# Performance work log

Measured on AMD Instinct MI355X. Metric: run time of the kernel, lower is better.

The kernel has to match this reference:

```python
import jax, jax.numpy as jnp
import numpy as np

DK = 128  # key/query head dim (also value dim)

def setup_inputs() -> dict:
    key = jax.random.key(0)
    k1, k2, k3, k4 = jax.random.split(key, 4)
    query = jax.random.normal(k1, (8, 512, 28, 28), dtype=jnp.float32)
    support = jax.random.normal(k2, (16, 512, 28, 28), dtype=jnp.float32)
    Wk = jax.random.normal(k3, (128, 512), dtype=jnp.float32) * (1.0 / np.sqrt(512.0))
    Wv = jax.random.normal(k4, (128, 512), dtype=jnp.float32) * (1.0 / np.sqrt(512.0))
    return {"query": query, "support": support, "Wk": Wk, "Wv": Wv}

def reference(query, support, Wk, Wv):
    B, D, H, W = query.shape
    N, Ds, Hs, Ws = support.shape
    q_flat = query.reshape(B, D, H * W)        # b d u
    s_flat = support.reshape(N, Ds, Hs * Ws)   # n d v
    # 1x1 convs == channel projections (query_head is aliased to key_head)
    q = jnp.einsum('kd,bdu->bku', Wk, q_flat)            # B dk u
    query_value = jnp.einsum('kd,bdu->bku', Wv, q_flat)  # B dv u
    support_key = jnp.einsum('kd,ndv->nkv', Wk, s_flat)  # N dk v
    support_value = jnp.einsum('kd,ndv->nkv', Wv, s_flat)  # N dv v
    scores = jnp.einsum('bku,nkv->bnuv', q, support_key) / jnp.sqrt(jnp.float32(DK))
    # first softmax over dim=3 in the source is dead code (overwritten); effective
    # attention is softmax over the support-class axis n (dim=1)
    attn = jax.nn.softmax(scores, axis=1)  # B N u v
    # note: u is summed out here, exactly as in the source einsum
    query_aligned = jnp.einsum('bnuv,nkv->bkv', attn, support_value)  # B dv v
    a = query_aligned.transpose(0, 2, 1)   # B v dv
    b = query_value.transpose(0, 2, 1)     # B u dv
    # cdist(p=2)**2 == squared euclidean distances; compute without forming diffs
    a2 = jnp.sum(a * a, axis=-1)  # B v
    b2 = jnp.sum(b * b, axis=-1)  # B u
    ab = jnp.einsum('bpd,brd->bpr', a, b)  # B v u
    d2 = jnp.maximum(a2[:, :, None] + b2[:, None, :] - 2.0 * ab, 0.0)
    P, R = d2.shape[1], d2.shape[2]
    return jnp.sum(d2, axis=(1, 2)) / (P * R)  # (B,)
```

## Files before the change

kernel.cpp:

```cpp
#include <hip/hip_runtime.h>

#define U_CNT 784
#define DKH   128
#define DD    512
#define NS    16

typedef short bf16x8 __attribute__((ext_vector_type(8)));
typedef float f32x4  __attribute__((ext_vector_type(4)));

__device__ __forceinline__ unsigned short f2bf(float f) {
  unsigned u = __builtin_bit_cast(unsigned, f);
  u += 0x7fffu + ((u >> 16) & 1u);
  return (unsigned short)(u >> 16);
}

__device__ __forceinline__ float rowg_sum(float x) {
  float a, b;
  asm("v_mov_b32 %0, %2\n\t"
      "v_mov_b32 %1, %2\n\t"
      "v_permlane16_swap_b32 %0, %1"
      : "=&v"(a), "=&v"(b) : "v"(x));
  float s = a + b;
  float c, d;
  asm("v_mov_b32 %0, %2\n\t"
      "v_mov_b32 %1, %2\n\t"
      "v_permlane32_swap_b32 %0, %1"
      : "=&v"(c), "=&v"(d) : "v"(s));
  return c + d;
}


__global__ __launch_bounds__(256)
void cast_w(const float* __restrict__ Wk, const float* __restrict__ Wv,
            unsigned short* __restrict__ Wkv_f) {
  int g = blockIdx.x * 256 + threadIdx.x;
  int fidx = g >> 6, l = g & 63;
  int f = fidx >> 4, rd = (fidx >> 2) & 3, ds = fidx & 3;
  int row = f * 16 + (l & 15);
  int dbase = rd * 128 + ds * 32 + (l >> 4) * 8;
  const float* src = (row < 128) ? (Wk + row * DD + dbase) : (Wv + (row - 128) * DD + dbase);
  unsigned short* dst = Wkv_f + (size_t)fidx * 512 + l * 8;
#pragma unroll
  for (int j = 0; j < 8; ++j) dst[j] = f2bf(src[j]);
}

__global__ __launch_bounds__(256, 1)
void proj_kernel(const float* __restrict__ query, const float* __restrict__ support,
                 const unsigned short* __restrict__ Wkv_f,
                 unsigned short* __restrict__ q_f, unsigned short* __restrict__ sk_f,
                 float* __restrict__ sv_t, float* __restrict__ S1p, float* __restrict__ S2p) {
  constexpr int PB = 112;
  constexpr int DR = 128;
  constexpr int RW = DR + 8;
  __shared__ __align__(16) unsigned short xs[2][PB * RW];
  int pc = blockIdx.x;
  int m  = blockIdx.y;
  int tid = threadIdx.x;
  int p0 = pc * PB;
  const float* X = (m < 8) ? (query + (size_t)m * DD * U_CNT)
                           : (support + (size_t)(m - 8) * DD * U_CNT);
  int drow = tid >> 1, pg = tid & 1;
  const float* xrow = X + p0 + pg * 4;

  float4 vbuf[14];
  auto loadR = [&](int rd) {
    const float* s = xrow + (size_t)(rd * DR + drow) * U_CNT;
#pragma unroll
    for (int i = 0; i < 14; ++i) vbuf[i] = *(const float4*)(s + i * 8);
  };
  auto storeR = [&](int bb) {
    unsigned short* d0 = &xs[bb][(pg * 4) * RW + drow];
#pragma unroll
    for (int i = 0; i < 14; ++i) {
      unsigned short* dp = d0 + (i * 8) * RW;
      dp[0]      = f2bf(vbuf[i].x); dp[RW]     = f2bf(vbuf[i].y);
      dp[2 * RW] = f2bf(vbuf[i].z); dp[3 * RW] = f2bf(vbuf[i].w);
    }
  };

  int wave = tid >> 6, l = tid & 63;
  int col = l & 15, rowg = l >> 4;

  f32x4 acc[7][4];
  f32x4 zero = {0.f, 0.f, 0.f, 0.f};
#pragma unroll
  for (int v7 = 0; v7 < 7; ++v7)
#pragma unroll
    for (int rr = 0; rr < 4; ++rr) acc[v7][rr] = zero;

  loadR(0); storeR(0);
  __syncthreads();
  for (int rd = 0; rd < 4; ++rd) {
    if (rd < 3) loadR(rd + 1);
    int bb = rd & 1;
#pragma unroll
    for (int ds = 0; ds < 4; ++ds) {
      int dl = ds * 32 + rowg * 8;
      bf16x8 Af[4];
#pragma unroll
      for (int rr = 0; rr < 4; ++rr)
        Af[rr] = *(const bf16x8*)(Wkv_f +
                 (size_t)((((wave * 4 + rr) * 4 + rd) * 4 + ds) * 512) + l * 8);
#pragma unroll
      for (int v7 = 0; v7 < 7; ++v7) {
        bf16x8 bf = *(const bf16x8*)(&xs[bb][(v7 * 16 + col) * RW + dl]);
#pragma unroll
        for (int rr = 0; rr < 4; ++rr)
          acc[v7][rr] = __builtin_amdgcn_mfma_f32_16x16x32_bf16(Af[rr], bf, acc[v7][rr], 0, 0, 0);
      }
    }
    if (rd < 3) {
      __syncthreads();
      storeR((rd + 1) & 1);
      __syncthreads();
    }
  }

  if (m < 8) {
    if (wave < 2) {
#pragma unroll
      for (int rr = 0; rr < 4; ++rr) {
        int r = wave * 4 + rr;
        const float sc = 0.08838834764831845f * 1.4426950408889634f;
#pragma unroll
        for (int v7 = 0; v7 < 7; ++v7) {
          ushort4 o;
          o.x = f2bf(acc[v7][rr][0] * sc); o.y = f2bf(acc[v7][rr][1] * sc);
          o.z = f2bf(acc[v7][rr][2] * sc); o.w = f2bf(acc[v7][rr][3] * sc);
          size_t off = (size_t)m * 100352 + (size_t)(pc * 7 + v7) * 2048 +
                       (size_t)(2 * r + (rowg >> 1)) * 128 + col * 8 + (rowg & 1) * 4;
          *(ushort4*)(q_f + off) = o;
        }
      }
    } else {
      float s1 = 0.f;
#pragma unroll
      for (int rr = 0; rr < 4; ++rr) {
        int r = wave * 4 + rr;
#pragma unroll
        for (int j = 0; j < 4; ++j) {
          float xsum = 0.f;
#pragma unroll
          for (int v7 = 0; v7 < 7; ++v7) {
            float x = acc[v7][rr][j];
            s1 += x * x; xsum += x;
          }
          xsum += __shfl_xor(xsum, 1, 64); xsum += __shfl_xor(xsum, 2, 64);
          xsum += __shfl_xor(xsum, 4, 64); xsum += __shfl_xor(xsum, 8, 64);
          if (col == 0)
            S2p[((size_t)pc * 8 + m) * DKH + (r - 8) * 16 + rowg * 4 + j] = xsum;
        }
      }
#pragma unroll
      for (int o = 32; o >= 1; o >>= 1) s1 += __shfl_xor(s1, o, 64);
      if (l == 0) S1p[((wave - 2) * 7 + pc) * 8 + m] = s1;
    }
  } else {
    int img = m - 8;
    if (wave < 2) {
#pragma unroll
      for (int rr = 0; rr < 4; ++rr) {
        int r = wave * 4 + rr;
#pragma unroll
        for (int v7 = 0; v7 < 7; ++v7) {
          ushort4 o;
          o.x = f2bf(acc[v7][rr][0]); o.y = f2bf(acc[v7][rr][1]);
          o.z = f2bf(acc[v7][rr][2]); o.w = f2bf(acc[v7][rr][3]);
          size_t off = (size_t)(p0 + v7 * 16 + col) * 2048 +
                       (size_t)(2 * r + (rowg >> 1)) * 128 + img * 8 + (rowg & 1) * 4;
          *(ushort4*)(sk_f + off) = o;
        }
      }
    } else {
#pragma unroll
      for (int rr = 0; rr < 4; ++rr) {
        int r = wave * 4 + rr;
        int kb = (r - 8) * 16 + rowg * 4;
#pragma unroll
        for (int v7 = 0; v7 < 7; ++v7) {
          int p = p0 + v7 * 16 + col;
          float4 o = make_float4(acc[v7][rr][0], acc[v7][rr][1], acc[v7][rr][2], acc[v7][rr][3]);
          *(float4*)(sv_t + (size_t)(img * U_CNT + p) * DKH + kb) = o;
        }
      }
    }
  }
}

__global__ __launch_bounds__(256, 3)
void score_kernel(const unsigned short* __restrict__ q_f,
                  const unsigned short* __restrict__ sk_f,
                  float* __restrict__ w_part) {
  int bx = blockIdx.x;
  int b  = bx & 7;
  int inner = bx >> 3;
  int uc = inner / 49;
  int vb = inner - uc * 49;
  int wv = threadIdx.x >> 6;
  int l  = threadIdx.x & 63;
  int col = l & 15, rowg = l >> 4;
  int vbase = vb * 16 + wv * 4;

  bf16x8 A[4][4];
#pragma unroll
  for (int v = 0; v < 4; ++v) {
    const unsigned short* ap = sk_f + (size_t)(vbase + v) * 2048 + rowg * 128 + col * 8;
#pragma unroll
    for (int s = 0; s < 4; ++s) A[v][s] = *(const bf16x8*)(ap + s * 512);
  }

  float wl[4][4];
#pragma unroll
  for (int v = 0; v < 4; ++v)
#pragma unroll
    for (int j = 0; j < 4; ++j) wl[v][j] = 0.f;

  int ut0 = (uc == 0) ? 0 : uc * 12 + 1;
  int cnt = (uc == 0) ? 13 : 12;
  const unsigned short* qb = q_f + (size_t)b * 100352 + rowg * 128 + col * 8;
  f32x4 zero = {0.f, 0.f, 0.f, 0.f};

  const unsigned short* qp0 = qb + (size_t)ut0 * 2048;
  bf16x8 B0 = *(const bf16x8*)(qp0);
  bf16x8 B1 = *(const bf16x8*)(qp0 + 512);
  bf16x8 B2 = *(const bf16x8*)(qp0 + 1024);
  bf16x8 B3 = *(const bf16x8*)(qp0 + 1536);

  for (int it = 0; it < cnt; ++it) {
    int nit = (it + 1 < cnt) ? it + 1 : it;
    const unsigned short* qp = qb + (size_t)(ut0 + nit) * 2048;
    bf16x8 N0 = *(const bf16x8*)(qp);
    bf16x8 N1 = *(const bf16x8*)(qp + 512);
    bf16x8 N2 = *(const bf16x8*)(qp + 1024);
    bf16x8 N3 = *(const bf16x8*)(qp + 1536);

    f32x4 acc[4];
#pragma unroll
    for (int v = 0; v < 4; ++v)
      acc[v] = __builtin_amdgcn_mfma_f32_16x16x32_bf16(A[v][0], B0, zero, 0, 0, 0);
#pragma unroll
    for (int v = 0; v < 4; ++v)
      acc[v] = __builtin_amdgcn_mfma_f32_16x16x32_bf16(A[v][1], B1, acc[v], 0, 0, 0);
#pragma unroll
    for (int v = 0; v < 4; ++v)
      acc[v] = __builtin_amdgcn_mfma_f32_16x16x32_bf16(A[v][2], B2, acc[v], 0, 0, 0);
#pragma unroll
    for (int v = 0; v < 4; ++v)
      acc[v] = __builtin_amdgcn_mfma_f32_16x16x32_bf16(A[v][3], B3, acc[v], 0, 0, 0);

    float e[4][4], ps[4];
#pragma unroll
    for (int v = 0; v < 4; ++v) {
      e[v][0] = __builtin_amdgcn_exp2f(acc[v][0]);
      e[v][1] = __builtin_amdgcn_exp2f(acc[v][1]);
      e[v][2] = __builtin_amdgcn_exp2f(acc[v][2]);
      e[v][3] = __builtin_amdgcn_exp2f(acc[v][3]);
      ps[v] = (e[v][0] + e[v][1]) + (e[v][2] + e[v][3]);
    }
#pragma unroll
    for (int v = 0; v < 4; ++v) ps[v] = rowg_sum(ps[v]);
#pragma unroll
    for (int v = 0; v < 4; ++v) {
      float r = __builtin_amdgcn_rcpf(ps[v]);
      wl[v][0] += e[v][0] * r; wl[v][1] += e[v][1] * r;
      wl[v][2] += e[v][2] * r; wl[v][3] += e[v][3] * r;
    }
    B0 = N0; B1 = N1; B2 = N2; B3 = N3;
  }
#pragma unroll
  for (int v = 0; v < 4; ++v)
#pragma unroll
    for (int j = 0; j < 4; ++j) {
      float x = wl[v][j];
      x += __shfl_xor(x, 1, 64); x += __shfl_xor(x, 2, 64);
      x += __shfl_xor(x, 4, 64); x += __shfl_xor(x, 8, 64);
      wl[v][j] = x;
    }
  __shared__ float wst[4][4][16];
#pragma unroll
  for (int v = 0; v < 4; ++v)
    if (col == v) {
#pragma unroll
      for (int j = 0; j < 4; ++j) wst[wv][v][rowg * 4 + j] = wl[v][j];
    }
  __syncthreads();
  int t = threadIdx.x;
  int vl = t >> 4, c = t & 15;
  w_part[(((size_t)uc * 8 + b) * U_CNT + vb * 16 + vl) * NS + c] =
      wst[vl >> 2][vl & 3][c];
}

__global__ __launch_bounds__(256)
void align_kernel(const float* __restrict__ w_part, const float* __restrict__ sv_t,
                  float* __restrict__ T1p, float* __restrict__ T2p) {
  int vt2 = blockIdx.x;
  int t = threadIdx.x;
  __shared__ float w_sh[2][8][16];
  {
    int vl = t >> 7, b = (t >> 4) & 7, n = t & 15;
    float s = 0.f;
#pragma unroll
    for (int uc = 0; uc < 4; ++uc)
      s += w_part[(((size_t)uc * 8 + b) * U_CNT + vt2 * 2 + vl) * NS + n];
    w_sh[vl][b][n] = s;
  }
  __syncthreads();
  int k = t & 127, vl = t >> 7;
  int v = vt2 * 2 + vl;
  float a[8];
#pragma unroll
  for (int b = 0; b < 8; ++b) a[b] = 0.f;
#pragma unroll
  for (int n = 0; n < NS; ++n) {
    float s = sv_t[((size_t)n * U_CNT + v) * DKH + k];
#pragma unroll
    for (int b = 0; b < 8; ++b) a[b] += w_sh[vl][b][n] * s;
  }
  __shared__ float red[8][128];
  if (vl == 1) {
#pragma unroll
    for (int b = 0; b < 8; ++b) red[b][k] = a[b];
  }
  __syncthreads();
  if (vl == 0) {
#pragma unroll
    for (int b = 0; b < 8; ++b)
      T2p[((size_t)vt2 * 8 + b) * DKH + k] = a[b] + red[b][k];
  }
  __shared__ float sw1[4][8];
#pragma unroll
  for (int b = 0; b < 8; ++b) {
    float x = a[b] * a[b];
#pragma unroll
    for (int o = 32; o >= 1; o >>= 1) x += __shfl_xor(x, o, 64);
    if ((t & 63) == 0) sw1[t >> 6][b] = x;
  }
  __syncthreads();
  if (t < 8) T1p[vt2 * 8 + t] = sw1[0][t] + sw1[1][t] + sw1[2][t] + sw1[3][t];
}

__global__ __launch_bounds__(256)
void reduce_partials(const float* __restrict__ S1p, const float* __restrict__ T1p,
                     const float* __restrict__ S2p, const float* __restrict__ T2p,
                     float* __restrict__ S2, float* __restrict__ T2,
                     float* __restrict__ ST1) {
  __shared__ float smem[264];
  int bx = blockIdx.x, t = threadIdx.x;
  if (bx < 32) {
    int b = bx >> 2, kq = bx & 3;
    int kl = t & 31, g = t >> 5;
    int k = kq * 32 + kl;
    float s = 0.f;
    for (int w = g; w < 392; w += 8)
      s += T2p[((size_t)w * 8 + b) * DKH + k];
    smem[g * 32 + kl] = s;
    __syncthreads();
    if (t < 32) {
      float v = 0.f;
#pragma unroll
      for (int g2 = 0; g2 < 8; ++g2) v += smem[g2 * 32 + t];
      T2[b * DKH + kq * 32 + t] = v;
    }
  } else {
    int b = bx - 32;
    int k = t & 127, h = t >> 7;
    float s = 0.f;
    for (int w = h; w < 7; w += 2)
      s += S2p[((size_t)w * 8 + b) * DKH + k];
    if (h == 1) smem[k] = s;
    __syncthreads();
    if (h == 0) S2[b * DKH + k] = s + smem[k];
    float c = 0.f;
    for (int i = t; i < 14; i += 256)  c += S1p[i * 8 + b];
    for (int i = t; i < 392; i += 256) c += T1p[i * 8 + b];
#pragma unroll
    for (int o = 32; o >= 1; o >>= 1) c += __shfl_xor(c, o, 64);
    if ((t & 63) == 0) smem[256 + (t >> 6)] = c;
    __syncthreads();
    if (t == 0) ST1[b] = smem[256] + smem[257] + smem[258] + smem[259];
  }
}

__global__ void final_kernel(const float* __restrict__ S2, const float* __restrict__ T2,
                             const float* __restrict__ ST1, float* __restrict__ out) {
  int b = blockIdx.x, t = threadIdx.x;
  float p = S2[b * DKH + t] * T2[b * DKH + t];
#pragma unroll
  for (int o = 32; o >= 1; o >>= 1) p += __shfl_xor(p, o, 64);
  __shared__ float s2[2];
  if ((t & 63) == 0) s2[t >> 6] = p;
  __syncthreads();
  if (t == 0)
    out[b] = (784.0f * ST1[b] - 2.0f * (s2[0] + s2[1])) * (1.0f / (784.0f * 784.0f));
}

extern "C" void kernel_launch(void* const* d_in, const int* in_sizes, int n_in,
                              void* d_out, int out_size, void* d_ws, size_t ws_size,
                              hipStream_t stream) {
  const float* query   = (const float*)d_in[0];
  const float* support = (const float*)d_in[1];
  const float* Wk      = (const float*)d_in[2];
  const float* Wv      = (const float*)d_in[3];
  float* out = (float*)d_out;
  char* ws = (char*)d_ws;

  unsigned short* Wkv  = (unsigned short*)(ws + 0);
  unsigned short* q_f  = (unsigned short*)(ws + 262144);
  unsigned short* sk_f = (unsigned short*)(ws + 1867776);
  float*          sv_t = (float*)(ws + 5079040);
  float*          w_part = (float*)(ws + 11501568);
  float*          S1p  = (float*)(ws + 14712832);
  float*          T1p  = (float*)(ws + 14716928);
  float*          S2p  = (float*)(ws + 14733312);
  float*          T2p  = (float*)(ws + 14934016);
  float*          S2   = (float*)(ws + 16539648);
  float*          T2   = (float*)(ws + 16543744);
  float*          ST1  = (float*)(ws + 16547840);
  if (ws_size < (size_t)16548000) return;

  cast_w<<<64, 256, 0, stream>>>(Wk, Wv, Wkv);
  proj_kernel<<<dim3(7, 24), 256, 0, stream>>>(query, support, Wkv, q_f, sk_f, sv_t, S1p, S2p);
  score_kernel<<<1568, 256, 0, stream>>>(q_f, sk_f, w_part);
  align_kernel<<<392, 256, 0, stream>>>(w_part, sv_t, T1p, T2p);
  reduce_partials<<<40, 256, 0, stream>>>(S1p, T1p, S2p, T2p, S2, T2, ST1);
  final_kernel<<<8, 128, 0, stream>>>(S2, T2, ST1, out);
}
```

Baseline: 153.1 us.

## Split input transpose and bf16 cast into separate kernel before projection

A new transpose_x kernel converts query/support to bf16 and transposes them to position-major layout in workspace. proj_kernel then reads B fragments straight from global memory and no longer does LDS staging, double buffering or its syncthreads. The goal is better parallelism for the transpose (1344 blocks instead of 168) and a simpler GEMM loop. The cost is an extra kernel launch, about 19MB of extra global traffic, and uncached strided global loads inside the MFMA loop.

Measured after the change: 167.5 us. +9.4%, slower.

```diff
diff --git a/kernel.cpp b/kernel.cpp
--- a/kernel.cpp
+++ b/kernel.cpp
@@ -44,42 +44,49 @@
   for (int j = 0; j < 8; ++j) dst[j] = f2bf(src[j]);
 }
 
+__global__ __launch_bounds__(256)
+void transpose_x(const float* __restrict__ query, const float* __restrict__ support,
+                 unsigned short* __restrict__ X_t) {
+  constexpr int TP = 112, TD = 64, LDT = TD + 8;
+  __shared__ __align__(16) unsigned short tl[TP * LDT];
+  int pc = blockIdx.x, dc = blockIdx.y, m = blockIdx.z;
+  const float* X = (m < 8) ? (query + (size_t)m * DD * U_CNT)
+                           : (support + (size_t)(m - 8) * DD * U_CNT);
+  int t = threadIdx.x;
+  int dl = t >> 2, pq = t & 3;
+  const float* src = X + (size_t)(dc * TD + dl) * U_CNT + pc * TP + pq * 4;
+#pragma unroll
+  for (int i = 0; i < 7; ++i) {
+    float4 v = *(const float4*)(src + i * 16);
+    unsigned short* d0 = &tl[(pq * 4 + i * 16) * LDT + dl];
+    d0[0]       = f2bf(v.x); d0[LDT]     = f2bf(v.y);
+    d0[2 * LDT] = f2bf(v.z); d0[3 * LDT] = f2bf(v.w);
+  }
+  __syncthreads();
+  int dl8 = (t & 7) * 8;
+#pragma unroll
+  for (int pass = 0; pass < 4; ++pass) {
+    int pl = (t >> 3) + pass * 32;
+    if (pl < TP) {
+      unsigned short* dst = X_t + (size_t)m * (U_CNT * DD) +
+                            (size_t)(pc * TP + pl) * DD + dc * TD + dl8;
+      *(bf16x8*)dst = *(const bf16x8*)(&tl[pl * LDT + dl8]);
+    }
+  }
+}
+
 __global__ __launch_bounds__(256, 1)
-void proj_kernel(const float* __restrict__ query, const float* __restrict__ support,
+void proj_kernel(const unsigned short* __restrict__ X_t,
                  const unsigned short* __restrict__ Wkv_f,
                  unsigned short* __restrict__ q_f, unsigned short* __restrict__ sk_f,
                  float* __restrict__ sv_t, float* __restrict__ S1p, float* __restrict__ S2p) {
-  constexpr int PB = 112;
-  constexpr int DR = 128;
-  constexpr int RW = DR + 8;
-  __shared__ __align__(16) unsigned short xs[2][PB * RW];
   int pc = blockIdx.x;
   int m  = blockIdx.y;
+  int p0 = pc * 112;
   int tid = threadIdx.x;
-  int p0 = pc * PB;
-  const float* X = (m < 8) ? (query + (size_t)m * DD * U_CNT)
-                           : (support + (size_t)(m - 8) * DD * U_CNT);
-  int drow = tid >> 1, pg = tid & 1;
-  const float* xrow = X + p0 + pg * 4;
-
-  float4 vbuf[14];
-  auto loadR = [&](int rd) {
-    const float* s = xrow + (size_t)(rd * DR + drow) * U_CNT;
-#pragma unroll
-    for (int i = 0; i < 14; ++i) vbuf[i] = *(const float4*)(s + i * 8);
-  };
-  auto storeR = [&](int bb) {
-    unsigned short* d0 = &xs[bb][(pg * 4) * RW + drow];
-#pragma unroll
-    for (int i = 0; i < 14; ++i) {
-      unsigned short* dp = d0 + (i * 8) * RW;
-      dp[0]      = f2bf(vbuf[i].x); dp[RW]     = f2bf(vbuf[i].y);
-      dp[2 * RW] = f2bf(vbuf[i].z); dp[3 * RW] = f2bf(vbuf[i].w);
-    }
-  };
-
   int wave = tid >> 6, l = tid & 63;
   int col = l & 15, rowg = l >> 4;
+  const unsigned short* Xb = X_t + (size_t)m * (U_CNT * DD);
 
   f32x4 acc[7][4];
   f32x4 zero = {0.f, 0.f, 0.f, 0.f};
@@ -88,11 +95,7 @@
 #pragma unroll
     for (int rr = 0; rr < 4; ++rr) acc[v7][rr] = zero;
 
-  loadR(0); storeR(0);
-  __syncthreads();
   for (int rd = 0; rd < 4; ++rd) {
-    if (rd < 3) loadR(rd + 1);
-    int bb = rd & 1;
 #pragma unroll
     for (int ds = 0; ds < 4; ++ds) {
       int dl = ds * 32 + rowg * 8;
@@ -103,16 +106,11 @@
                  (size_t)((((wave * 4 + rr) * 4 + rd) * 4 + ds) * 512) + l * 8);
 #pragma unroll
       for (int v7 = 0; v7 < 7; ++v7) {
-        bf16x8 bf = *(const bf16x8*)(&xs[bb][(v7 * 16 + col) * RW + dl]);
+        bf16x8 bf = *(const bf16x8*)(Xb + (size_t)(p0 + v7 * 16 + col) * DD + rd * 128 + dl);
 #pragma unroll
         for (int rr = 0; rr < 4; ++rr)
           acc[v7][rr] = __builtin_amdgcn_mfma_f32_16x16x32_bf16(Af[rr], bf, acc[v7][rr], 0, 0, 0);
       }
-    }
-    if (rd < 3) {
-      __syncthreads();
-      storeR((rd + 1) & 1);
-      __syncthreads();
     }
   }
 
@@ -405,21 +403,23 @@
   char* ws = (char*)d_ws;
 
   unsigned short* Wkv  = (unsigned short*)(ws + 0);
-  unsigned short* q_f  = (unsigned short*)(ws + 262144);
-  unsigned short* sk_f = (unsigned short*)(ws + 1867776);
-  float*          sv_t = (float*)(ws + 5079040);
-  float*          w_part = (float*)(ws + 11501568);
-  float*          S1p  = (float*)(ws + 14712832);
-  float*          T1p  = (float*)(ws + 14716928);
-  float*          S2p  = (float*)(ws + 14733312);
-  float*          T2p  = (float*)(ws + 14934016);
-  float*          S2   = (float*)(ws + 16539648);
-  float*          T2   = (float*)(ws + 16543744);
-  float*          ST1  = (float*)(ws + 16547840);
-  if (ws_size < (size_t)16548000) return;
+  unsigned short* X_t  = (unsigned short*)(ws + 262144);
+  unsigned short* q_f  = (unsigned short*)(ws + 19529728);
+  unsigned short* sk_f = (unsigned short*)(ws + 21135360);
+  float*          sv_t = (float*)(ws + 24346624);
+  float*          w_part = (float*)(ws + 30769152);
+  float*          S1p  = (float*)(ws + 32374784);
+  float*          T1p  = (float*)(ws + 32378880);
+  float*          S2p  = (float*)(ws + 32391424);
+  float*          T2p  = (float*)(ws + 32420096);
+  float*          S2   = (float*)(ws + 34025728);
+  float*          T2   = (float*)(ws + 34029824);
+  float*          ST1  = (float*)(ws + 34033920);
+  if (ws_size < (size_t)34034176) return;
 
   cast_w<<<64, 256, 0, stream>>>(Wk, Wv, Wkv);
-  proj_kernel<<<dim3(7, 24), 256, 0, stream>>>(query, support, Wkv, q_f, sk_f, sv_t, S1p, S2p);
+  transpose_x<<<dim3(7, 8, 24), 256, 0, stream>>>(query, support, X_t);
+  proj_kernel<<<dim3(7, 24), 256, 0, stream>>>(X_t, Wkv, q_f, sk_f, sv_t, S1p, S2p);
   score_kernel<<<1568, 256, 0, stream>>>(q_f, sk_f, w_part);
   align_kernel<<<392, 256, 0, stream>>>(w_part, sv_t, T1p, T2p);
   reduce_partials<<<40, 256, 0, stream>>>(S1p, T1p, S2p, T2p, S2, T2, ST1);
```
